# Kernel optimization log

Measured on AMD Instinct MI355X. Metric: run time of the kernel, lower is better.

Reference implementation:

```python
import jax, jax.numpy as jnp
import numpy as np

V, E, H, T = 100000, 256, 256, 8192


def setup_inputs() -> dict:
    key = jax.random.key(0)
    k0, k1, k2, k3, k4, k5 = jax.random.split(key, 6)
    s = 1.0 / np.sqrt(H)  # PyTorch LSTM init bound
    tokens = jax.random.randint(k0, (T,), 0, V)
    embedding = jax.random.normal(k1, (V, E), jnp.float32) * 0.02
    W_ih = jax.random.uniform(k2, (4 * H, E), jnp.float32, -s, s)
    W_hh = jax.random.uniform(k3, (4 * H, H), jnp.float32, -s, s)
    b_ih = jax.random.uniform(k4, (4 * H,), jnp.float32, -s, s)
    b_hh = jax.random.uniform(k5, (4 * H,), jnp.float32, -s, s)
    return {"tokens": tokens, "embedding": embedding, "W_ih": W_ih,
            "W_hh": W_hh, "b_ih": b_ih, "b_hh": b_hh}


def reference(tokens, embedding, W_ih, W_hh, b_ih, b_hh):
    # Flattened tree traversal: one embed + one LSTM cell step per token,
    # hidden state threaded through, all per-token hiddens collected.
    emb = embedding[tokens]                      # [T, E] gather (memory-bound)
    # precompute input contribution for every step (batched GEMM)
    xg = emb @ W_ih.T + (b_ih + b_hh)            # [T, 4H]

    def step(carry, xg_t):
        h, c = carry
        g = xg_t + W_hh @ h                      # [4H]
        i, f, gg, o = jnp.split(g, 4)
        i = jax.nn.sigmoid(i)
        f = jax.nn.sigmoid(f)
        gg = jnp.tanh(gg)
        o = jax.nn.sigmoid(o)
        c = f * c + i * gg
        h = o * jnp.tanh(c)
        return (h, c), h

    h0 = jnp.zeros((H,), emb.dtype)
    c0 = jnp.zeros((H,), emb.dtype)
    (h_last, c_last), hiddens = jax.lax.scan(step, (h0, c0), xg)
    return hiddens, h_last, c_last
```

## Files before the change

### kernel.cpp

```cpp
#include <hip/hip_runtime.h>

#define T_STEPS 8192
#define HID 256
#define NBLK 128
#define THREADS 256
#define SPIN_T0   4096
#define SPIN_RUN  64
#define SLOW_N    6
#define SLOW_CAP  512

#define MAGIC_READY 0x13579BDFu
#define EMPTY_XCD   0xFFFFFFFFu
#define DONE_MAGIC  0x600DD00Eu

__device__ __forceinline__ float tanh_fast(float x) { return 2.0f / (1.0f + __expf(-2.0f * x)) - 1.0f; }

__device__ __forceinline__ void st_u64_sc0(unsigned long long* p, unsigned long long v) {
    asm volatile("global_store_dwordx2 %0, %1, off sc0" :: "v"(p), "v"(v) : "memory");
}
__device__ __forceinline__ void inv_l1() {
    asm volatile("buffer_inv sc0" ::: "memory");
}
__device__ __forceinline__ void ld4_issue_sc0(const unsigned long long* p,
                                              unsigned long long& a, unsigned long long& b,
                                              unsigned long long& c, unsigned long long& d) {
    asm volatile(
        "global_load_dwordx2 %0, %4, off sc0\n\t"
        "global_load_dwordx2 %1, %4, off offset:8 sc0\n\t"
        "global_load_dwordx2 %2, %4, off offset:16 sc0\n\t"
        "global_load_dwordx2 %3, %4, off offset:24 sc0"
        : "=&v"(a), "=&v"(b), "=&v"(c), "=&v"(d)
        : "v"(p) : "memory");
}
__device__ __forceinline__ void vm_wait1_bind(unsigned long long& a, unsigned long long& b,
                                              unsigned long long& c, unsigned long long& d) {
    asm volatile("s_waitcnt vmcnt(1)" ::: "memory");
    __builtin_amdgcn_sched_barrier(0);
    asm volatile("" : "+v"(a), "+v"(b), "+v"(c), "+v"(d));
}
__device__ __forceinline__ void vm_wait0_bind(unsigned long long& a, unsigned long long& b,
                                              unsigned long long& c, unsigned long long& d) {
    asm volatile("s_waitcnt vmcnt(0)" ::: "memory");
    __builtin_amdgcn_sched_barrier(0);
    asm volatile("" : "+v"(a), "+v"(b), "+v"(c), "+v"(d));
}

__global__ __launch_bounds__(THREADS, 1)
void lstm_scan(const int* __restrict__ tokens,
               const float* __restrict__ emb,
               const float* __restrict__ Wih,
               const float* __restrict__ Whh,
               const float* __restrict__ bih,
               const float* __restrict__ bhh,
               float* __restrict__ out,
               unsigned long long* __restrict__ hbL,
               unsigned long long* __restrict__ hbA,
               unsigned* __restrict__ ctl)
{
    __shared__ int s_role;
    if (threadIdx.x == 0) {
        unsigned xcc;
        asm volatile("s_getreg_b32 %0, hwreg(HW_REG_XCC_ID, 0, 4)" : "=s"(xcc));
        unsigned* ready   = ctl + 0;
        unsigned* elected = ctl + 1;
        unsigned* cnt     = ctl + 2;
        if (blockIdx.x == 0) {
            for (int i = 0; i < 8; ++i)
                __hip_atomic_store(cnt + i, 0u, __ATOMIC_RELAXED, __HIP_MEMORY_SCOPE_AGENT);
            __hip_atomic_store(elected, EMPTY_XCD, __ATOMIC_RELAXED, __HIP_MEMORY_SCOPE_AGENT);
            __hip_atomic_store(ctl + 10, 0u, __ATOMIC_RELAXED, __HIP_MEMORY_SCOPE_AGENT);
            __hip_atomic_store(ready, MAGIC_READY, __ATOMIC_RELEASE, __HIP_MEMORY_SCOPE_AGENT);
        }
        while (__hip_atomic_load(ready, __ATOMIC_ACQUIRE, __HIP_MEMORY_SCOPE_AGENT) != MAGIC_READY)
            asm volatile("s_sleep 1");
        unsigned r = __hip_atomic_fetch_add(cnt + xcc, 1u, __ATOMIC_RELAXED, __HIP_MEMORY_SCOPE_AGENT);
        if (r == 15u) {
            unsigned expv = EMPTY_XCD;
            __hip_atomic_compare_exchange_strong(elected, &expv, xcc,
                __ATOMIC_RELAXED, __ATOMIC_RELAXED, __HIP_MEMORY_SCOPE_AGENT);
        }
        unsigned e;
        while ((e = __hip_atomic_load(elected, __ATOMIC_ACQUIRE, __HIP_MEMORY_SCOPE_AGENT)) == EMPTY_XCD)
            asm volatile("s_sleep 1");
        s_role = (xcc == e && r < 16u) ? (int)r : -1;
    }
    __syncthreads();
    const int w = s_role;

    if (w < 0) {
        float x0 = 1.0f, x1 = 2.0f, x2 = 3.0f, x3 = 4.0f;
        const float a = 1.0000001f, b = 1e-7f;
        const unsigned* done = ctl + 10;
        for (;;) {
            #pragma unroll 64
            for (int i = 0; i < 512; ++i) {
                x0 = fmaf(x0, a, b); x1 = fmaf(x1, a, b);
                x2 = fmaf(x2, a, b); x3 = fmaf(x3, a, b);
            }
            if (__hip_atomic_load(done, __ATOMIC_RELAXED, __HIP_MEMORY_SCOPE_AGENT) == DONE_MAGIC)
                break;
        }
        asm volatile("" :: "v"(x0 + x1 + x2 + x3));
        return;
    }

    const int tid  = threadIdx.x;
    const int lane = tid & 63;
    const int wave = tid >> 6;
    const int rl   = lane >> 2;
    const int kq   = lane & 3;
    const int r_wg = wave * 16 + rl;
    const int unit_local = r_wg >> 2;
    const int gate = r_wg & 3;
    const int unit = w * 16 + unit_local;
    const int grow = gate * 256 + unit;
    const int kbase = kq * 64;

    float whh[64], wih[64];
    {
        const float* p = Whh + (size_t)grow * 256 + kbase;
        #pragma unroll
        for (int j = 0; j < 64; j += 4) {
            float4 q = *(const float4*)(p + j);
            whh[j] = q.x; whh[j+1] = q.y; whh[j+2] = q.z; whh[j+3] = q.w;
        }
        p = Wih + (size_t)grow * 256 + kbase;
        #pragma unroll
        for (int j = 0; j < 64; j += 4) {
            float4 q = *(const float4*)(p + j);
            wih[j] = q.x; wih[j+1] = q.y; wih[j+2] = q.z; wih[j+3] = q.w;
        }
    }
    const float bias = bih[grow] + bhh[grow];
    const bool owner = ((lane & 15) == 0);
    const float act_scale = (gate == 2) ? 2.0f : 1.0f;
    const float act_off   = (gate == 2) ? 1.0f : 0.0f;

    __shared__ float4 lds_h4[4][17];
    __shared__ float4 lds_e4[2][4][17];

    if (owner) {
        st_u64_sc0(hbL + unit, 0ull);
        __hip_atomic_store(hbA + unit, 0ull, __ATOMIC_RELAXED, __HIP_MEMORY_SCOPE_AGENT);
    }
    if (wave == 1) {
        int tk = tokens[0];
        float4 e = *(const float4*)(emb + (size_t)tk * 256 + lane * 4);
        lds_e4[0][lane >> 4][lane & 15] = e;
    }
    float c = 0.0f;
    bool useL2 = true;
    int  slow  = 0;
    unsigned long long pk_prev = 0ull;
    __syncthreads();

    for (int t = 0; t < T_STEPS; ++t) {
        if (wave == 1) {
            int tk = tokens[(t + 1 < T_STEPS) ? t + 1 : t];
            float4 e = *(const float4*)(emb + (size_t)tk * 256 + lane * 4);
            lds_e4[(t + 1) & 1][lane >> 4][lane & 15] = e;
        }
        unsigned long long* hbp = hbL + (size_t)(t & 1) * 256 + lane * 4;
        unsigned long long q0, q1, q2, q3;
        if (wave == 0) {
            if (useL2) {
                inv_l1();
                ld4_issue_sc0(hbp, q0, q1, q2, q3);
            }
            if (owner)
                __hip_atomic_store(hbA + (size_t)(t & 1) * 256 + unit, pk_prev,
                                   __ATOMIC_RELAXED, __HIP_MEMORY_SCOPE_AGENT);
        }
        float aA = 0.0f, aB = 0.0f, aC = 0.0f, aD = 0.0f;
        {
            const float4* eb = lds_e4[t & 1][kq];
            #pragma unroll
            for (int i = 0; i < 16; i += 4) {
                float4 v0 = eb[i], v1 = eb[i+1], v2 = eb[i+2], v3 = eb[i+3];
                aA = fmaf(wih[4*i+ 0], v0.x, aA); aA = fmaf(wih[4*i+ 1], v0.y, aA);
                aA = fmaf(wih[4*i+ 2], v0.z, aA); aA = fmaf(wih[4*i+ 3], v0.w, aA);
                aB = fmaf(wih[4*i+ 4], v1.x, aB); aB = fmaf(wih[4*i+ 5], v1.y, aB);
                aB = fmaf(wih[4*i+ 6], v1.z, aB); aB = fmaf(wih[4*i+ 7], v1.w, aB);
                aC = fmaf(wih[4*i+ 8], v2.x, aC); aC = fmaf(wih[4*i+ 9], v2.y, aC);
                aC = fmaf(wih[4*i+10], v2.z, aC); aC = fmaf(wih[4*i+11], v2.w, aC);
                aD = fmaf(wih[4*i+12], v3.x, aD); aD = fmaf(wih[4*i+13], v3.y, aD);
                aD = fmaf(wih[4*i+14], v3.z, aD); aD = fmaf(wih[4*i+15], v3.w, aD);
            }
        }
        if (wave == 0) {
            const unsigned int tt = (unsigned int)t;
            bool got = false;
            if (useL2) {
                vm_wait1_bind(q0, q1, q2, q3);
                const int smax = (t == 0) ? SPIN_T0 : SPIN_RUN;
                int n = 0;
                for (;;) {
                    if (((unsigned int)(q0 >> 32) == tt) & ((unsigned int)(q1 >> 32) == tt) &
                        ((unsigned int)(q2 >> 32) == tt) & ((unsigned int)(q3 >> 32) == tt)) {
                        got = true; break;
                    }
                    if (++n > smax) { useL2 = false; break; }
                    inv_l1();
                    ld4_issue_sc0(hbp, q0, q1, q2, q3);
                    vm_wait0_bind(q0, q1, q2, q3);
                }
                if (got && t > 0 && n > SLOW_N && ++slow > SLOW_CAP) useL2 = false;
            }
            if (!got) {
                const unsigned long long* ha = hbA + (size_t)(t & 1) * 256 + lane * 4;
                for (;;) {
                    q0 = __hip_atomic_load(ha + 0, __ATOMIC_RELAXED, __HIP_MEMORY_SCOPE_AGENT);
                    q1 = __hip_atomic_load(ha + 1, __ATOMIC_RELAXED, __HIP_MEMORY_SCOPE_AGENT);
                    q2 = __hip_atomic_load(ha + 2, __ATOMIC_RELAXED, __HIP_MEMORY_SCOPE_AGENT);
                    q3 = __hip_atomic_load(ha + 3, __ATOMIC_RELAXED, __HIP_MEMORY_SCOPE_AGENT);
                    if (((unsigned int)(q0 >> 32) == tt) & ((unsigned int)(q1 >> 32) == tt) &
                        ((unsigned int)(q2 >> 32) == tt) & ((unsigned int)(q3 >> 32) == tt))
                        break;
                }
            }
            union { unsigned int i; float f; } a, b, cc, d;
            a.i = (unsigned int)q0; b.i = (unsigned int)q1;
            cc.i = (unsigned int)q2; d.i = (unsigned int)q3;
            lds_h4[lane >> 4][lane & 15] = make_float4(a.f, b.f, cc.f, d.f);
        }
        __syncthreads();
        {
            const float4* hq = lds_h4[kq];
            #pragma unroll
            for (int i = 0; i < 16; i += 4) {
                float4 v0 = hq[i], v1 = hq[i+1], v2 = hq[i+2], v3 = hq[i+3];
                aA = fmaf(whh[4*i+ 0], v0.x, aA); aA = fmaf(whh[4*i+ 1], v0.y, aA);
                aA = fmaf(whh[4*i+ 2], v0.z, aA); aA = fmaf(whh[4*i+ 3], v0.w, aA);
                aB = fmaf(whh[4*i+ 4], v1.x, aB); aB = fmaf(whh[4*i+ 5], v1.y, aB);
                aB = fmaf(whh[4*i+ 6], v1.z, aB); aB = fmaf(whh[4*i+ 7], v1.w, aB);
                aC = fmaf(whh[4*i+ 8], v2.x, aC); aC = fmaf(whh[4*i+ 9], v2.y, aC);
                aC = fmaf(whh[4*i+10], v2.z, aC); aC = fmaf(whh[4*i+11], v2.w, aC);
                aD = fmaf(whh[4*i+12], v3.x, aD); aD = fmaf(whh[4*i+13], v3.y, aD);
                aD = fmaf(whh[4*i+14], v3.z, aD); aD = fmaf(whh[4*i+15], v3.w, aD);
            }
        }
        float acc = (aA + aB) + (aC + aD);
        acc += __shfl_xor(acc, 1, 64);
        acc += __shfl_xor(acc, 2, 64);
        acc += bias;
        float ex = __expf(-act_scale * acc);
        float av = act_scale / (1.0f + ex) - act_off;
        const int base = lane & 48;
        float fv = __shfl(av, base + 4,  64);
        float gv = __shfl(av, base + 8,  64);
        float ov = __shfl(av, base + 12, 64);
        if (owner) {
            c = fmaf(fv, c, av * gv);
            float h_out = ov * tanh_fast(c);
            union { unsigned int i; float f; } u; u.f = h_out;
            unsigned long long pk =
                (((unsigned long long)(unsigned int)(t + 1)) << 32) | (unsigned long long)u.i;
            const size_t so = (size_t)((t + 1) & 1) * 256 + unit;
            st_u64_sc0(hbL + so, pk);
            if (wave == 0) pk_prev = pk;
            else __hip_atomic_store(hbA + so, pk, __ATOMIC_RELAXED,
                                    __HIP_MEMORY_SCOPE_AGENT);
            out[(size_t)t * HID + unit] = h_out;
            if (t == T_STEPS - 1) {
                out[(size_t)T_STEPS * HID + unit]       = h_out;
                out[(size_t)T_STEPS * HID + HID + unit] = c;
            }
        }
    }

    if (w == 0 && tid == 0) {
        __hip_atomic_store(ctl + 10, DONE_MAGIC, __ATOMIC_RELEASE, __HIP_MEMORY_SCOPE_AGENT);
        __hip_atomic_store(ctl + 0, 0u, __ATOMIC_RELAXED, __HIP_MEMORY_SCOPE_AGENT);
    }
}

extern "C" void kernel_launch(void* const* d_in, const int* in_sizes, int n_in,
                              void* d_out, int out_size, void* d_ws, size_t ws_size,
                              hipStream_t stream) {
    const int*   tokens = (const int*)d_in[0];
    const float* emb    = (const float*)d_in[1];
    const float* Wih    = (const float*)d_in[2];
    const float* Whh    = (const float*)d_in[3];
    const float* bih    = (const float*)d_in[4];
    const float* bhh    = (const float*)d_in[5];
    float* out = (float*)d_out;
    unsigned long long* hbL = (unsigned long long*)d_ws;
    unsigned long long* hbA = (unsigned long long*)((char*)d_ws + 4096);
    unsigned* ctl = (unsigned*)((char*)d_ws + 8192);

    lstm_scan<<<NBLK, THREADS, 0, stream>>>(tokens, emb, Wih, Whh, bih, bhh, out, hbL, hbA, ctl);
}
```

Baseline: 11.77 ms.

## Dedicate a fifth poller wave to hidden-state exchange and pipeline embedding loads

Adds a fifth wave that only polls the cross-block hidden-state buffers and publishes h into double-buffered LDS, so the four compute waves no longer carry the spin-wait. Tokens are staged in shared memory, and embedding rows are prefetched two steps ahead with hand-managed vmcnt waits. The L2-to-atomic fallback logic gets a separate failure counter, and the first-step spin budget is raised. The cost is an extra wave per block and fragile manual waitcnt accounting.

New measurement: 16.85 ms. 43.2% more time.

```diff
diff --git a/kernel.cpp b/kernel.cpp
--- a/kernel.cpp
+++ b/kernel.cpp
@@ -3,24 +3,25 @@
 #define T_STEPS 8192
 #define HID 256
 #define NBLK 128
-#define THREADS 256
-#define SPIN_T0   4096
-#define SPIN_RUN  64
-#define SLOW_N    6
-#define SLOW_CAP  512
+#define THREADS 320
+#define SPIN_T0  16384
+#define SPIN_RUN 64
+#define SLOW_N   8
+#define SLOW_CAP 512
+#define FB_CAP   256
 
 #define MAGIC_READY 0x13579BDFu
 #define EMPTY_XCD   0xFFFFFFFFu
 #define DONE_MAGIC  0x600DD00Eu
 
+typedef float v4f __attribute__((ext_vector_type(4)));
+
 __device__ __forceinline__ float tanh_fast(float x) { return 2.0f / (1.0f + __expf(-2.0f * x)) - 1.0f; }
 
 __device__ __forceinline__ void st_u64_sc0(unsigned long long* p, unsigned long long v) {
     asm volatile("global_store_dwordx2 %0, %1, off sc0" :: "v"(p), "v"(v) : "memory");
 }
-__device__ __forceinline__ void inv_l1() {
-    asm volatile("buffer_inv sc0" ::: "memory");
-}
+__device__ __forceinline__ void inv_l1() { asm volatile("buffer_inv sc0" ::: "memory"); }
 __device__ __forceinline__ void ld4_issue_sc0(const unsigned long long* p,
                                               unsigned long long& a, unsigned long long& b,
                                               unsigned long long& c, unsigned long long& d) {
@@ -32,17 +33,19 @@
         : "=&v"(a), "=&v"(b), "=&v"(c), "=&v"(d)
         : "v"(p) : "memory");
 }
-__device__ __forceinline__ void vm_wait1_bind(unsigned long long& a, unsigned long long& b,
-                                              unsigned long long& c, unsigned long long& d) {
-    asm volatile("s_waitcnt vmcnt(1)" ::: "memory");
-    __builtin_amdgcn_sched_barrier(0);
-    asm volatile("" : "+v"(a), "+v"(b), "+v"(c), "+v"(d));
-}
 __device__ __forceinline__ void vm_wait0_bind(unsigned long long& a, unsigned long long& b,
                                               unsigned long long& c, unsigned long long& d) {
     asm volatile("s_waitcnt vmcnt(0)" ::: "memory");
     __builtin_amdgcn_sched_barrier(0);
     asm volatile("" : "+v"(a), "+v"(b), "+v"(c), "+v"(d));
+}
+__device__ __forceinline__ void ld_e4_issue(const float* p, v4f& e) {
+    asm volatile("global_load_dwordx4 %0, %1, off" : "=v"(e) : "v"(p) : "memory");
+}
+__device__ __forceinline__ bool tags_ok(unsigned long long a, unsigned long long b,
+                                        unsigned long long c, unsigned long long d, unsigned tt) {
+    return ((unsigned)(a >> 32) == tt) & ((unsigned)(b >> 32) == tt) &
+           ((unsigned)(c >> 32) == tt) & ((unsigned)(d >> 32) == tt);
 }
 
 __global__ __launch_bounds__(THREADS, 1)
@@ -107,104 +110,35 @@
     const int tid  = threadIdx.x;
     const int lane = tid & 63;
     const int wave = tid >> 6;
-    const int rl   = lane >> 2;
-    const int kq   = lane & 3;
-    const int r_wg = wave * 16 + rl;
-    const int unit_local = r_wg >> 2;
-    const int gate = r_wg & 3;
-    const int unit = w * 16 + unit_local;
-    const int grow = gate * 256 + unit;
-    const int kbase = kq * 64;
-
-    float whh[64], wih[64];
-    {
-        const float* p = Whh + (size_t)grow * 256 + kbase;
-        #pragma unroll
-        for (int j = 0; j < 64; j += 4) {
-            float4 q = *(const float4*)(p + j);
-            whh[j] = q.x; whh[j+1] = q.y; whh[j+2] = q.z; whh[j+3] = q.w;
-        }
-        p = Wih + (size_t)grow * 256 + kbase;
-        #pragma unroll
-        for (int j = 0; j < 64; j += 4) {
-            float4 q = *(const float4*)(p + j);
-            wih[j] = q.x; wih[j+1] = q.y; wih[j+2] = q.z; wih[j+3] = q.w;
-        }
-    }
-    const float bias = bih[grow] + bhh[grow];
-    const bool owner = ((lane & 15) == 0);
-    const float act_scale = (gate == 2) ? 2.0f : 1.0f;
-    const float act_off   = (gate == 2) ? 1.0f : 0.0f;
-
-    __shared__ float4 lds_h4[4][17];
-    __shared__ float4 lds_e4[2][4][17];
-
-    if (owner) {
-        st_u64_sc0(hbL + unit, 0ull);
-        __hip_atomic_store(hbA + unit, 0ull, __ATOMIC_RELAXED, __HIP_MEMORY_SCOPE_AGENT);
-    }
-    if (wave == 1) {
-        int tk = tokens[0];
-        float4 e = *(const float4*)(emb + (size_t)tk * 256 + lane * 4);
-        lds_e4[0][lane >> 4][lane & 15] = e;
-    }
-    float c = 0.0f;
-    bool useL2 = true;
-    int  slow  = 0;
-    unsigned long long pk_prev = 0ull;
+
+    __shared__ v4f lds_h[2][4][17];
+    __shared__ v4f lds_e[2][4][17];
+    __shared__ __align__(16) int s_tok[T_STEPS];
+
+    for (int i = tid; i < T_STEPS / 4; i += THREADS)
+        *(int4*)&s_tok[i * 4] = *(const int4*)&tokens[i * 4];
     __syncthreads();
 
-    for (int t = 0; t < T_STEPS; ++t) {
-        if (wave == 1) {
-            int tk = tokens[(t + 1 < T_STEPS) ? t + 1 : t];
-            float4 e = *(const float4*)(emb + (size_t)tk * 256 + lane * 4);
-            lds_e4[(t + 1) & 1][lane >> 4][lane & 15] = e;
-        }
-        unsigned long long* hbp = hbL + (size_t)(t & 1) * 256 + lane * 4;
-        unsigned long long q0, q1, q2, q3;
-        if (wave == 0) {
-            if (useL2) {
-                inv_l1();
-                ld4_issue_sc0(hbp, q0, q1, q2, q3);
-            }
-            if (owner)
-                __hip_atomic_store(hbA + (size_t)(t & 1) * 256 + unit, pk_prev,
-                                   __ATOMIC_RELAXED, __HIP_MEMORY_SCOPE_AGENT);
-        }
-        float aA = 0.0f, aB = 0.0f, aC = 0.0f, aD = 0.0f;
-        {
-            const float4* eb = lds_e4[t & 1][kq];
-            #pragma unroll
-            for (int i = 0; i < 16; i += 4) {
-                float4 v0 = eb[i], v1 = eb[i+1], v2 = eb[i+2], v3 = eb[i+3];
-                aA = fmaf(wih[4*i+ 0], v0.x, aA); aA = fmaf(wih[4*i+ 1], v0.y, aA);
-                aA = fmaf(wih[4*i+ 2], v0.z, aA); aA = fmaf(wih[4*i+ 3], v0.w, aA);
-                aB = fmaf(wih[4*i+ 4], v1.x, aB); aB = fmaf(wih[4*i+ 5], v1.y, aB);
-                aB = fmaf(wih[4*i+ 6], v1.z, aB); aB = fmaf(wih[4*i+ 7], v1.w, aB);
-                aC = fmaf(wih[4*i+ 8], v2.x, aC); aC = fmaf(wih[4*i+ 9], v2.y, aC);
-                aC = fmaf(wih[4*i+10], v2.z, aC); aC = fmaf(wih[4*i+11], v2.w, aC);
-                aD = fmaf(wih[4*i+12], v3.x, aD); aD = fmaf(wih[4*i+13], v3.y, aD);
-                aD = fmaf(wih[4*i+14], v3.z, aD); aD = fmaf(wih[4*i+15], v3.w, aD);
-            }
-        }
-        if (wave == 0) {
-            const unsigned int tt = (unsigned int)t;
+    if (wave == 4) {
+        __syncthreads();
+        bool useL2 = true; int slow = 0, fb = 0;
+        for (int t = 0; t < T_STEPS; ++t) {
+            const unsigned tt = (unsigned)t;
+            unsigned long long* hbp = hbL + (size_t)(t & 1) * 256 + lane * 4;
+            unsigned long long q0, q1, q2, q3;
             bool got = false;
             if (useL2) {
-                vm_wait1_bind(q0, q1, q2, q3);
                 const int smax = (t == 0) ? SPIN_T0 : SPIN_RUN;
                 int n = 0;
                 for (;;) {
-                    if (((unsigned int)(q0 >> 32) == tt) & ((unsigned int)(q1 >> 32) == tt) &
-                        ((unsigned int)(q2 >> 32) == tt) & ((unsigned int)(q3 >> 32) == tt)) {
-                        got = true; break;
-                    }
-                    if (++n > smax) { useL2 = false; break; }
                     inv_l1();
                     ld4_issue_sc0(hbp, q0, q1, q2, q3);
                     vm_wait0_bind(q0, q1, q2, q3);
-                }
-                if (got && t > 0 && n > SLOW_N && ++slow > SLOW_CAP) useL2 = false;
+                    if (tags_ok(q0, q1, q2, q3, tt)) { got = true; break; }
+                    if (++n > smax) break;
+                }
+                if (!got) { if (++fb > FB_CAP) useL2 = false; }
+                else if (t > 0 && n > SLOW_N) { if (++slow > SLOW_CAP) useL2 = false; }
             }
             if (!got) {
                 const unsigned long long* ha = hbA + (size_t)(t & 1) * 256 + lane * 4;
@@ -213,57 +147,124 @@
                     q1 = __hip_atomic_load(ha + 1, __ATOMIC_RELAXED, __HIP_MEMORY_SCOPE_AGENT);
                     q2 = __hip_atomic_load(ha + 2, __ATOMIC_RELAXED, __HIP_MEMORY_SCOPE_AGENT);
                     q3 = __hip_atomic_load(ha + 3, __ATOMIC_RELAXED, __HIP_MEMORY_SCOPE_AGENT);
-                    if (((unsigned int)(q0 >> 32) == tt) & ((unsigned int)(q1 >> 32) == tt) &
-                        ((unsigned int)(q2 >> 32) == tt) & ((unsigned int)(q3 >> 32) == tt))
-                        break;
-                }
-            }
-            union { unsigned int i; float f; } a, b, cc, d;
-            a.i = (unsigned int)q0; b.i = (unsigned int)q1;
-            cc.i = (unsigned int)q2; d.i = (unsigned int)q3;
-            lds_h4[lane >> 4][lane & 15] = make_float4(a.f, b.f, cc.f, d.f);
-        }
+                    if (tags_ok(q0, q1, q2, q3, tt)) break;
+                }
+            }
+            union { unsigned i; float f; } ua, ub, uc, ud;
+            ua.i = (unsigned)q0; ub.i = (unsigned)q1; uc.i = (unsigned)q2; ud.i = (unsigned)q3;
+            v4f hv; hv[0] = ua.f; hv[1] = ub.f; hv[2] = uc.f; hv[3] = ud.f;
+            lds_h[t & 1][lane >> 4][lane & 15] = hv;
+            __syncthreads();
+        }
+    } else {
+        const int rl   = lane >> 2;
+        const int kq   = lane & 3;
+        const int r_wg = wave * 16 + rl;
+        const int unit = w * 16 + (r_wg >> 2);
+        const int gate = r_wg & 3;
+        const int grow = gate * 256 + unit;
+        const int kbase = kq * 64;
+
+        float whh[64], wih[64];
+        {
+            const float* p = Whh + (size_t)grow * 256 + kbase;
+            #pragma unroll
+            for (int j = 0; j < 64; j += 4) {
+                float4 q = *(const float4*)(p + j);
+                whh[j] = q.x; whh[j+1] = q.y; whh[j+2] = q.z; whh[j+3] = q.w;
+            }
+            p = Wih + (size_t)grow * 256 + kbase;
+            #pragma unroll
+            for (int j = 0; j < 64; j += 4) {
+                float4 q = *(const float4*)(p + j);
+                wih[j] = q.x; wih[j+1] = q.y; wih[j+2] = q.z; wih[j+3] = q.w;
+            }
+        }
+        const float bias = bih[grow] + bhh[grow];
+        const bool owner = ((lane & 15) == 0);
+        const float act_scale = (gate == 2) ? 2.0f : 1.0f;
+        const float act_off   = (gate == 2) ? 1.0f : 0.0f;
+
+        v4f e_pipe;
+        if (wave == 1) {
+            v4f e0 = *(const v4f*)(emb + (size_t)s_tok[0] * 256 + lane * 4);
+            lds_e[0][lane >> 4][lane & 15] = e0;
+            ld_e4_issue(emb + (size_t)s_tok[1] * 256 + lane * 4, e_pipe);
+        }
+        if (owner) {
+            st_u64_sc0(hbL + unit, 0ull);
+            __hip_atomic_store(hbA + unit, 0ull, __ATOMIC_RELAXED, __HIP_MEMORY_SCOPE_AGENT);
+        }
+        float c = 0.0f;
         __syncthreads();
-        {
-            const float4* hq = lds_h4[kq];
-            #pragma unroll
-            for (int i = 0; i < 16; i += 4) {
-                float4 v0 = hq[i], v1 = hq[i+1], v2 = hq[i+2], v3 = hq[i+3];
-                aA = fmaf(whh[4*i+ 0], v0.x, aA); aA = fmaf(whh[4*i+ 1], v0.y, aA);
-                aA = fmaf(whh[4*i+ 2], v0.z, aA); aA = fmaf(whh[4*i+ 3], v0.w, aA);
-                aB = fmaf(whh[4*i+ 4], v1.x, aB); aB = fmaf(whh[4*i+ 5], v1.y, aB);
-                aB = fmaf(whh[4*i+ 6], v1.z, aB); aB = fmaf(whh[4*i+ 7], v1.w, aB);
-                aC = fmaf(whh[4*i+ 8], v2.x, aC); aC = fmaf(whh[4*i+ 9], v2.y, aC);
-                aC = fmaf(whh[4*i+10], v2.z, aC); aC = fmaf(whh[4*i+11], v2.w, aC);
-                aD = fmaf(whh[4*i+12], v3.x, aD); aD = fmaf(whh[4*i+13], v3.y, aD);
-                aD = fmaf(whh[4*i+14], v3.z, aD); aD = fmaf(whh[4*i+15], v3.w, aD);
-            }
-        }
-        float acc = (aA + aB) + (aC + aD);
-        acc += __shfl_xor(acc, 1, 64);
-        acc += __shfl_xor(acc, 2, 64);
-        acc += bias;
-        float ex = __expf(-act_scale * acc);
-        float av = act_scale / (1.0f + ex) - act_off;
-        const int base = lane & 48;
-        float fv = __shfl(av, base + 4,  64);
-        float gv = __shfl(av, base + 8,  64);
-        float ov = __shfl(av, base + 12, 64);
-        if (owner) {
-            c = fmaf(fv, c, av * gv);
-            float h_out = ov * tanh_fast(c);
-            union { unsigned int i; float f; } u; u.f = h_out;
-            unsigned long long pk =
-                (((unsigned long long)(unsigned int)(t + 1)) << 32) | (unsigned long long)u.i;
-            const size_t so = (size_t)((t + 1) & 1) * 256 + unit;
-            st_u64_sc0(hbL + so, pk);
-            if (wave == 0) pk_prev = pk;
-            else __hip_atomic_store(hbA + so, pk, __ATOMIC_RELAXED,
-                                    __HIP_MEMORY_SCOPE_AGENT);
-            out[(size_t)t * HID + unit] = h_out;
-            if (t == T_STEPS - 1) {
-                out[(size_t)T_STEPS * HID + unit]       = h_out;
-                out[(size_t)T_STEPS * HID + HID + unit] = c;
+
+        for (int t = 0; t < T_STEPS; ++t) {
+            if (wave == 1) {
+                if (t == 0) { asm volatile("s_waitcnt vmcnt(2)" ::: "memory"); }
+                else        { asm volatile("s_waitcnt vmcnt(3)" ::: "memory"); }
+                __builtin_amdgcn_sched_barrier(0);
+                asm volatile("" : "+v"(e_pipe));
+                lds_e[(t + 1) & 1][lane >> 4][lane & 15] = e_pipe;
+                int nt = t + 2; if (nt > T_STEPS - 1) nt = T_STEPS - 1;
+                ld_e4_issue(emb + (size_t)s_tok[nt] * 256 + lane * 4, e_pipe);
+            }
+            float aA = 0.0f, aB = 0.0f, aC = 0.0f, aD = 0.0f;
+            {
+                const v4f* eb = &lds_e[t & 1][kq][0];
+                #pragma unroll
+                for (int i = 0; i < 16; i += 4) {
+                    v4f v0 = eb[i], v1 = eb[i+1], v2 = eb[i+2], v3 = eb[i+3];
+                    aA = fmaf(wih[4*i+ 0], v0[0], aA); aA = fmaf(wih[4*i+ 1], v0[1], aA);
+                    aA = fmaf(wih[4*i+ 2], v0[2], aA); aA = fmaf(wih[4*i+ 3], v0[3], aA);
+                    aB = fmaf(wih[4*i+ 4], v1[0], aB); aB = fmaf(wih[4*i+ 5], v1[1], aB);
+                    aB = fmaf(wih[4*i+ 6], v1[2], aB); aB = fmaf(wih[4*i+ 7], v1[3], aB);
+                    aC = fmaf(wih[4*i+ 8], v2[0], aC); aC = fmaf(wih[4*i+ 9], v2[1], aC);
+                    aC = fmaf(wih[4*i+10], v2[2], aC); aC = fmaf(wih[4*i+11], v2[3], aC);
+                    aD = fmaf(wih[4*i+12], v3[0], aD); aD = fmaf(wih[4*i+13], v3[1], aD);
+                    aD = fmaf(wih[4*i+14], v3[2], aD); aD = fmaf(wih[4*i+15], v3[3], aD);
+                }
+            }
+            __syncthreads();
+            {
+                const v4f* hq = &lds_h[t & 1][kq][0];
+                #pragma unroll
+                for (int i = 0; i < 16; i += 4) {
+                    v4f v0 = hq[i], v1 = hq[i+1], v2 = hq[i+2], v3 = hq[i+3];
+                    aA = fmaf(whh[4*i+ 0], v0[0], aA); aA = fmaf(whh[4*i+ 1], v0[1], aA);
+                    aA = fmaf(whh[4*i+ 2], v0[2], aA); aA = fmaf(whh[4*i+ 3], v0[3], aA);
+                    aB = fmaf(whh[4*i+ 4], v1[0], aB); aB = fmaf(whh[4*i+ 5], v1[1], aB);
+                    aB = fmaf(whh[4*i+ 6], v1[2], aB); aB = fmaf(whh[4*i+ 7], v1[3], aB);
+                    aC = fmaf(whh[4*i+ 8], v2[0], aC); aC = fmaf(whh[4*i+ 9], v2[1], aC);
+                    aC = fmaf(whh[4*i+10], v2[2], aC); aC = fmaf(whh[4*i+11], v2[3], aC);
+                    aD = fmaf(whh[4*i+12], v3[0], aD); aD = fmaf(whh[4*i+13], v3[1], aD);
+                    aD = fmaf(whh[4*i+14], v3[2], aD); aD = fmaf(whh[4*i+15], v3[3], aD);
+                }
+            }
+            float acc = (aA + aB) + (aC + aD);
+            acc += __shfl_xor(acc, 1, 64);
+            acc += __shfl_xor(acc, 2, 64);
+            acc += bias;
+            float ex = __expf(-act_scale * acc);
+            float av = act_scale / (1.0f + ex) - act_off;
+            const int base = lane & 48;
+            float fv = __shfl(av, base + 4,  64);
+            float gv = __shfl(av, base + 8,  64);
+            float ov = __shfl(av, base + 12, 64);
+            if (owner) {
+                c = fmaf(fv, c, av * gv);
+                float h = ov * tanh_fast(c);
+                union { unsigned i; float f; } u; u.f = h;
+                unsigned long long pk =
+                    (((unsigned long long)(unsigned)(t + 1)) << 32) | (unsigned long long)u.i;
+                const size_t so = (size_t)((t + 1) & 1) * 256 + unit;
+                st_u64_sc0(hbL + so, pk);
+                __hip_atomic_store(hbA + so, pk, __ATOMIC_RELAXED,
+                                   __HIP_MEMORY_SCOPE_AGENT);
+                out[(size_t)t * HID + unit] = h;
+                if (t == T_STEPS - 1) {
+                    out[(size_t)T_STEPS * HID + unit]       = h;
+                    out[(size_t)T_STEPS * HID + HID + unit] = c;
+                }
             }
         }
     }
```
